# Performance work log

Measured on AMD Instinct MI355X. Metric: run time of the kernel, lower is better.

The kernel has to match this reference:

```python
import jax, jax.numpy as jnp
import numpy as np

NQ = 20          # qubits
NLAYERS = 2
OUT_DIM = 512    # gen_output_dim (= zdim)
COND_DIM = 1
QOUT = min(NQ, OUT_DIM)  # = 20
BATCH = 262144


def _apply_ry(state, theta, w):
    # state: (2,)*NQ real tensor; RY = [[c,-s],[s,c]], c=cos(th/2), s=sin(th/2)
    c = jnp.cos(theta * 0.5)
    s = jnp.sin(theta * 0.5)
    st = jnp.moveaxis(state, w, 0)
    a0, a1 = st[0], st[1]
    st = jnp.stack([c * a0 - s * a1, s * a0 + c * a1])
    return jnp.moveaxis(st, 0, w)


def _apply_cz(state, w):
    # CZ on wires (w, w+1): flip sign where both bits are 1
    st = jnp.moveaxis(state, (w, w + 1), (0, 1))
    st = st.at[1, 1].multiply(-1.0)
    return jnp.moveaxis(st, (0, 1), (w, w + 1))


def _simulate(params):
    # Exact statevector simulation; all gates are real so state stays real.
    state = jnp.zeros((2,) * NQ, dtype=params.dtype).at[(0,) * NQ].set(1.0)
    for layer in range(NLAYERS):
        for w in range(NQ):
            state = _apply_ry(state, params[layer, w], w)
        for w in range(NQ - 1):
            state = _apply_cz(state, w)
    probs = state * state  # (2,)*NQ
    outs = []
    for w in range(QOUT):
        p = jnp.moveaxis(probs, w, 0).reshape(2, -1).sum(axis=1)
        outs.append(p[0] - p[1])  # <Z_w> = P(0) - P(1)
    return jnp.stack(outs)  # (QOUT,)


def setup_inputs() -> dict:
    key = jax.random.key(0)
    k1, k2, k3, k4 = jax.random.split(key, 4)
    cond_batch = jax.random.normal(k1, (BATCH, COND_DIM), dtype=jnp.float32)
    params = 0.05 * jax.random.normal(k2, (NLAYERS, NQ), dtype=jnp.float32)
    fan_in = QOUT + COND_DIM
    bound = 1.0 / np.sqrt(fan_in)
    W = jax.random.uniform(k3, (OUT_DIM, fan_in), jnp.float32, -bound, bound)
    b = jax.random.uniform(k4, (OUT_DIM,), jnp.float32, -bound, bound)
    return {"cond_batch": cond_batch, "params": params, "W": W, "b": b}


def reference(cond_batch, params, W, b):
    # The original qnode ignores `cond`, so the circuit output is identical
    # for every sample in the batch: compute once, broadcast.
    qout = _simulate(params)  # (QOUT,)
    outs = jnp.broadcast_to(qout, (cond_batch.shape[0], QOUT))
    x = jnp.concatenate([outs, cond_batch], axis=1)  # (B, QOUT+COND_DIM)
    return jnp.tanh(x @ W.T + b)  # (B, OUT_DIM)
```

## Files before the change

### kernel.cpp

```cpp
#include <hip/hip_runtime.h>
#include <math.h>

#define NQ 20
#define OUT_DIM 512
#define FAN_IN 21
#define BATCH 262144
#define GRID 2048

typedef float vfloat4 __attribute__((ext_vector_type(4)));

__global__ __launch_bounds__(OUT_DIM)
void prep_kernel(const float* __restrict__ params,
                 const float* __restrict__ W,
                 const float* __restrict__ b,
                 float* __restrict__ base,
                 float* __restrict__ wlast)
{
    __shared__ float qout[NQ];
    const int j = threadIdx.x;
    if (j < NQ) {
        float p0 = params[j];
        float p1 = params[NQ + j];
        float cl = (j > 0)      ? cosf(params[j - 1]) : 1.0f;
        float cr = (j < NQ - 1) ? cosf(params[j + 1]) : 1.0f;
        qout[j] = cosf(p0) * cosf(p1) - sinf(p0) * sinf(p1) * cl * cr;
    }
    __syncthreads();

    const float* wr = W + j * FAN_IN;
    float acc = b[j];
#pragma unroll
    for (int k = 0; k < NQ; ++k) acc += qout[k] * wr[k];
    base[j]  = acc;
    wlast[j] = wr[NQ];
}

__device__ __forceinline__ float ftanh(float x) {
    x = fminf(fmaxf(x, -10.0f), 10.0f);
    float e = __expf(2.0f * x);
    return 1.0f - 2.0f / (e + 1.0f);
}

__global__ __launch_bounds__(256)
void main_kernel(const float* __restrict__ cond,
                 const float* __restrict__ base,
                 const float* __restrict__ wlast,
                 float* __restrict__ out)
{
    const int t    = threadIdx.x;
    const int half = t >> 7;
    const int j    = (t & 127) << 2;

    const vfloat4 bs = *reinterpret_cast<const vfloat4*>(base  + j);
    const vfloat4 wl = *reinterpret_cast<const vfloat4*>(wlast + j);

    const int CHUNK = BATCH / GRID;
    const int row0  = blockIdx.x * CHUNK + half;

#pragma unroll 4
    for (int r = 0; r < CHUNK; r += 2) {
        const int row = row0 + r;
        const float c = cond[row];
        vfloat4 o;
        o.x = ftanh(fmaf(c, wl.x, bs.x));
        o.y = ftanh(fmaf(c, wl.y, bs.y));
        o.z = ftanh(fmaf(c, wl.z, bs.z));
        o.w = ftanh(fmaf(c, wl.w, bs.w));
        __builtin_nontemporal_store(o,
            reinterpret_cast<vfloat4*>(out + (size_t)row * OUT_DIM + j));
    }
}

extern "C" void kernel_launch(void* const* d_in, const int* in_sizes, int n_in,
                              void* d_out, int out_size, void* d_ws, size_t ws_size,
                              hipStream_t stream)
{
    const float* cond   = (const float*)d_in[0];
    const float* params = (const float*)d_in[1];
    const float* W      = (const float*)d_in[2];
    const float* b      = (const float*)d_in[3];
    float* out = (float*)d_out;

    float* base  = (float*)d_ws;
    float* wlast = base + OUT_DIM;

    prep_kernel<<<1, OUT_DIM, 0, stream>>>(params, W, b, base, wlast);
    main_kernel<<<GRID, 256, 0, stream>>>(cond, base, wlast, out);
}
```

Before: 115.7 us.

## Fuse prep and main kernels, recompute bias per block, simplify tanh

Removes the separate single-block prep kernel. Each of the 2048 blocks now recomputes the circuit expectation values and the 512-wide base/weight vectors from W and b, and stages its 128 cond values in shared memory. Tanh drops the clamp and uses a reciprocal with the factor 2 folded into the coefficients. Output stores change from nontemporal to regular. This saves one launch and the serial dependency between kernels, at the cost of redundant per-block W reads and trig work, plus possible NaN-free overflow behavior relying on rcp of inf.

```diff
diff --git a/kernel.cpp b/kernel.cpp
--- a/kernel.cpp
+++ b/kernel.cpp
@@ -9,65 +9,56 @@
 
 typedef float vfloat4 __attribute__((ext_vector_type(4)));
 
-__global__ __launch_bounds__(OUT_DIM)
-void prep_kernel(const float* __restrict__ params,
-                 const float* __restrict__ W,
-                 const float* __restrict__ b,
-                 float* __restrict__ base,
-                 float* __restrict__ wlast)
+__global__ __launch_bounds__(256)
+void fused_kernel(const float* __restrict__ cond,
+                  const float* __restrict__ params,
+                  const float* __restrict__ W,
+                  const float* __restrict__ b,
+                  float* __restrict__ out)
 {
     __shared__ float qout[NQ];
-    const int j = threadIdx.x;
-    if (j < NQ) {
-        float p0 = params[j];
-        float p1 = params[NQ + j];
-        float cl = (j > 0)      ? cosf(params[j - 1]) : 1.0f;
-        float cr = (j < NQ - 1) ? cosf(params[j + 1]) : 1.0f;
-        qout[j] = cosf(p0) * cosf(p1) - sinf(p0) * sinf(p1) * cl * cr;
+    __shared__ float sc[128];
+
+    const int t = threadIdx.x;
+    const int blk = blockIdx.x;
+
+    if (t < 128) sc[t] = cond[blk * 128 + t];
+    if (t < NQ) {
+        float p0 = params[t];
+        float p1 = params[NQ + t];
+        float cl = (t > 0)      ? cosf(params[t - 1]) : 1.0f;
+        float cr = (t < NQ - 1) ? cosf(params[t + 1]) : 1.0f;
+        qout[t] = cosf(p0) * cosf(p1) - sinf(p0) * sinf(p1) * cl * cr;
     }
     __syncthreads();
 
-    const float* wr = W + j * FAN_IN;
-    float acc = b[j];
-#pragma unroll
-    for (int k = 0; k < NQ; ++k) acc += qout[k] * wr[k];
-    base[j]  = acc;
-    wlast[j] = wr[NQ];
-}
-
-__device__ __forceinline__ float ftanh(float x) {
-    x = fminf(fmaxf(x, -10.0f), 10.0f);
-    float e = __expf(2.0f * x);
-    return 1.0f - 2.0f / (e + 1.0f);
-}
-
-__global__ __launch_bounds__(256)
-void main_kernel(const float* __restrict__ cond,
-                 const float* __restrict__ base,
-                 const float* __restrict__ wlast,
-                 float* __restrict__ out)
-{
-    const int t    = threadIdx.x;
     const int half = t >> 7;
     const int j    = (t & 127) << 2;
 
-    const vfloat4 bs = *reinterpret_cast<const vfloat4*>(base  + j);
-    const vfloat4 wl = *reinterpret_cast<const vfloat4*>(wlast + j);
+    vfloat4 A, B;
+#pragma unroll
+    for (int r = 0; r < 4; ++r) {
+        const float* wr = W + (j + r) * FAN_IN;
+        float acc = b[j + r];
+#pragma unroll
+        for (int k = 0; k < NQ; ++k) acc += qout[k] * wr[k];
+        B[r] = 2.0f * acc;
+        A[r] = 2.0f * wr[NQ];
+    }
 
-    const int CHUNK = BATCH / GRID;
-    const int row0  = blockIdx.x * CHUNK + half;
+    float* p = out + (size_t)(blk * 128 + half) * OUT_DIM + j;
 
-#pragma unroll 4
-    for (int r = 0; r < CHUNK; r += 2) {
-        const int row = row0 + r;
-        const float c = cond[row];
+#pragma unroll 8
+    for (int r = 0; r < 64; ++r) {
+        const float c = sc[2 * r + half];
         vfloat4 o;
-        o.x = ftanh(fmaf(c, wl.x, bs.x));
-        o.y = ftanh(fmaf(c, wl.y, bs.y));
-        o.z = ftanh(fmaf(c, wl.z, bs.z));
-        o.w = ftanh(fmaf(c, wl.w, bs.w));
-        __builtin_nontemporal_store(o,
-            reinterpret_cast<vfloat4*>(out + (size_t)row * OUT_DIM + j));
+#pragma unroll
+        for (int q = 0; q < 4; ++q) {
+            float e = __expf(fmaf(c, A[q], B[q]));
+            o[q] = fmaf(-2.0f, __frcp_rn(e + 1.0f), 1.0f);
+        }
+        *reinterpret_cast<vfloat4*>(p) = o;
+        p += 2 * OUT_DIM;
     }
 }
 
@@ -81,9 +72,5 @@
     const float* b      = (const float*)d_in[3];
     float* out = (float*)d_out;
 
-    float* base  = (float*)d_ws;
-    float* wlast = base + OUT_DIM;
-
-    prep_kernel<<<1, OUT_DIM, 0, stream>>>(params, W, b, base, wlast);
-    main_kernel<<<GRID, 256, 0, stream>>>(cond, base, wlast, out);
+    fused_kernel<<<GRID, 256, 0, stream>>>(cond, params, W, b, out);
 }
```

Result: faster. 111.5 us (-3.6%).
